# Optimization experiments

Hardware: AMD Instinct MI355X
Metric: run time of the kernel (lower is better)

The kernel has to match this reference:

```python
import jax, jax.numpy as jnp
import numpy as np

B, T, NS, NC, M = 256, 128, 12, 4, 6
MU = 0.1                 # barrier parameter alg.mu
REG_BASE = 1.6           # fp.reg_exp_base
REG = 2.0                # bp.reg
REG_FAC = REG_BASE ** REG - 1.0


def _mt(a):
    return jnp.swapaxes(a, -1, -2)


def setup_inputs():
    key = jax.random.key(0)
    k = jax.random.split(key, 18)
    rn = lambda i, shape: jax.random.normal(k[i], shape, dtype=jnp.float32)
    eye_s = jnp.eye(NS, dtype=jnp.float32)
    eye_c = jnp.eye(NC, dtype=jnp.float32)
    fx = 0.9 * eye_s + 0.02 * rn(0, (B, T, NS, NS))
    fu = 0.1 * rn(1, (B, T, NS, NC))
    fxx = 0.01 * rn(2, (B, T, NS, NS, NS))
    fxu = 0.01 * rn(3, (B, T, NS, NS, NC))
    fuu = 0.01 * rn(4, (B, T, NS, NC, NC))
    qx = 0.1 * rn(5, (B, T, NS))
    qu = 0.1 * rn(6, (B, T, NC))
    Ax = 0.1 * rn(7, (B, T, NS, NS))
    qxx = eye_s + Ax @ _mt(Ax)            # PSD stage cost Hessian
    Au = 0.1 * rn(8, (B, T, NC, NC))
    quu = eye_c + Au @ _mt(Au)            # PD control Hessian
    qxu = 0.05 * rn(9, (B, T, NS, NC))
    cx = 0.1 * rn(10, (B, T, M, NS))
    cu = 0.1 * rn(11, (B, T, M, NC))
    # feasible iterate: c < 0 strictly, dual s > 0
    c = -(jax.random.uniform(k[12], (B, T, M), dtype=jnp.float32) + 0.1)
    s = 0.05 + 0.1 * jax.random.uniform(k[13], (B, T, M), dtype=jnp.float32)
    px = 0.1 * rn(14, (B, NS))
    P = 0.1 * rn(15, (B, NS, NS))
    pxx = eye_s + P @ _mt(P)              # PSD terminal Hessian
    return {"qx": qx, "qu": qu, "qxx": qxx, "qxu": qxu, "quu": quu,
            "fx": fx, "fu": fu, "fxx": fxx, "fxu": fxu, "fuu": fuu,
            "cx": cx, "cu": cu, "c": c, "s": s, "px": px, "pxx": pxx}


def _backward_pass(qx, qu, qxx, qxu, quu, fx, fu, fxx, fxu, fuu, cx, cu, c, s, px, pxx):
    """Feasible-branch ipddp Riccati backward recursion over T steps, batched over B."""
    Bsz = qx.shape[0]

    def step(carry, inp):
        Vx, Vxx, dV0, dV1, qu_err, mu_err = carry
        (qx_t, qu_t, qxx_t, qxu_t, quu_t, fx_t, fu_t,
         fxx_t, fxu_t, fuu_t, cx_t, cu_t, c_t, s_t) = inp
        s_col = s_t[..., None]                      # (B,M,1)
        c_col = c_t[..., None]                      # (B,M,1)
        # Q-function expansions
        Qx = qx_t[..., None] + _mt(cx_t) @ s_col + _mt(fx_t) @ Vx       # (B,NS,1)
        Qu = qu_t[..., None] + _mt(cu_t) @ s_col + _mt(fu_t) @ Vx       # (B,NC,1)
        fxV = _mt(fx_t) @ Vxx
        v = Vx[..., 0]                              # (B,NS)
        Qxx = qxx_t + fxV @ fx_t + jnp.einsum('bs,bsij->bij', v, fxx_t)
        Qxu = qxu_t + fxV @ fu_t + jnp.einsum('bs,bsij->bij', v, fxu_t)
        Quu = quu_t + _mt(fu_t) @ Vxx @ fu_t + jnp.einsum('bs,bsij->bij', v, fuu_t)
        Quu = 0.5 * (Quu + _mt(Quu))
        Quu_reg = Quu + quu_t * REG_FAC
        # interior-point (feasible) modifications
        r = s_col * c_col + MU                      # (B,M,1)
        cinv = 1.0 / c_col
        sc = (s_t / c_t)[..., None]                 # diag(SCinv) entries
        SCcu = sc * cu_t                            # SCinv @ cu
        SCcx = sc * cx_t                            # SCinv @ cx
        cuSCcu = _mt(cu_t) @ SCcu
        Qu = Qu - _mt(cu_t) @ (cinv * r)
        tempQux = _mt(Qxu) - _mt(cu_t) @ SCcx       # (B,NC,NS)
        rhs = jnp.concatenate([Qu, tempQux], axis=-1)   # (B,NC,1+NS)
        kK = -jnp.linalg.solve(Quu_reg - cuSCcu, rhs)
        ku = kK[..., :1]                            # (B,NC,1)
        Ku = kK[..., 1:]                            # (B,NC,NS)
        cuku = cu_t @ ku                            # (B,M,1)
        ks = (-cinv * (r + s_col * cuku))[..., 0]   # (B,M)
        Ks = -(sc * (cx_t + cu_t @ Ku))             # (B,M,NS)
        Quu2 = Quu - cuSCcu
        Qxu2 = _mt(tempQux)
        Qxx2 = Qxx - _mt(cx_t) @ SCcx
        Qx2 = Qx - _mt(cx_t) @ (cinv * r)
        dV0 = dV0 + (_mt(ku) @ Qu)[..., 0, 0]
        dV1 = dV1 + 0.5 * (_mt(ku) @ Quu2 @ ku)[..., 0, 0]
        QxuKu = Qxu2 @ Ku
        KtQ = _mt(Ku) @ Quu2
        Vx_new = Qx2 + _mt(Ku) @ Qu + KtQ @ ku + Qxu2 @ ku
        Vxx_new = Qxx2 + _mt(QxuKu) + QxuKu + KtQ @ Ku
        Vxx_new = 0.5 * (Vxx_new + _mt(Vxx_new))
        qu_err = jnp.maximum(qu_err, jnp.max(jnp.abs(Qu)))
        mu_err = jnp.maximum(mu_err, jnp.max(jnp.abs(r)))
        return (Vx_new, Vxx_new, dV0, dV1, qu_err, mu_err), (ku[..., 0], Ku, ks, Ks)

    xs = tuple(jnp.moveaxis(a, 1, 0) for a in
               (qx, qu, qxx, qxu, quu, fx, fu, fxx, fxu, fuu, cx, cu, c, s))
    zero = jnp.zeros((), jnp.float32)
    init = (px[..., None], pxx, jnp.zeros((Bsz,), jnp.float32),
            jnp.zeros((Bsz,), jnp.float32), zero, zero)
    carry, outs = jax.lax.scan(step, init, xs, reverse=True)
    Vx, Vxx, dV0, dV1, qu_err, mu_err = carry
    ku, Ku, ks, Ks = (jnp.moveaxis(o, 0, 1) for o in outs)
    dV = jnp.stack([dV0, dV1], axis=-1)             # (B,2)
    opterr = jnp.maximum(qu_err, mu_err)            # c_err == 0 in feasible branch
    return ku, Ku, ks, Ks, dV, opterr, Vx[..., 0], Vxx


def reference(qx, qu, qxx, qxu, quu, fx, fu, fxx, fxu, fuu, cx, cu, c, s, px, pxx):
    return _backward_pass(qx, qu, qxx, qxu, quu, fx, fu, fxx, fxu, fuu,
                          cx, cu, c, s, px, pxx)
```

## Files before the change

kernel.cpp:

```cpp
#include <hip/hip_runtime.h>
#include <cstdint>
#include <cstddef>

#define B_  256
#define T_  128

constexpr float MU_F      = 0.1f;
constexpr float REG_FAC_F = (float)(1.6 * 1.6 - 1.0);

#define OF_FX   0
#define OF_FU   144
#define OF_FXX  192
#define OF_FXU  1920
#define OF_FUU  2496
#define OF_QXX  2688
#define OF_QXU  2832
#define OF_QUU  2880
#define OF_QX   2896
#define OF_QU   2908
#define OF_CX   2912
#define OF_CU   2984
#define OF_C    3008
#define OF_S    3014
#define STG_N   3020

#define O_KU    0
#define O_KUBIG 131072
#define O_KS    1703936
#define O_KSBIG 1900544
#define O_DV    4259840
#define O_OPT   4260352
#define O_VX    4260353
#define O_VXX   4263425

__device__ __forceinline__ void gl_lds16(const float* g, float* l) {
    __builtin_amdgcn_global_load_lds((const __attribute__((address_space(1))) void*)g,
                                     (__attribute__((address_space(3))) void*)l, 16, 0, 0);
}
__device__ __forceinline__ void gl_lds4(const float* g, float* l) {
    __builtin_amdgcn_global_load_lds((const __attribute__((address_space(1))) void*)g,
                                     (__attribute__((address_space(3))) void*)l, 4, 0, 0);
}
__device__ __forceinline__ void wait_vm0() {
    asm volatile("s_waitcnt vmcnt(0)" ::: "memory");
}

__global__ __launch_bounds__(64) void ddp_backward(
    const float* __restrict__ qx,  const float* __restrict__ qu,
    const float* __restrict__ qxx, const float* __restrict__ qxu,
    const float* __restrict__ quu, const float* __restrict__ fx,
    const float* __restrict__ fu,  const float* __restrict__ fxx,
    const float* __restrict__ fxu, const float* __restrict__ fuu,
    const float* __restrict__ cx,  const float* __restrict__ cu,
    const float* __restrict__ c_,  const float* __restrict__ s_,
    const float* __restrict__ px,  const float* __restrict__ pxx,
    float* __restrict__ out, float* __restrict__ ws)
{
    const int lane = threadIdx.x;
    const int b    = blockIdx.x;

    __shared__ float stg[2][STG_N];
    __shared__ float sVx[12], sVxx[144];
    __shared__ float sfxV[144], sfuV[48];
    __shared__ float sQxx2[144], stQux[48], sGuu[16];
    __shared__ float sQxb[12], sQub[4], sQu[4], sQx2[12];
    __shared__ float sr[6], scinv[6], ssc[6], sscr[6];
    __shared__ float sKu[48], sku[4];
    __shared__ float sErr[2];

    float accDV0 = 0.f, accDV1 = 0.f, accQE = 0.f, accME = 0.f;

    const float* srcs[14] = {qx, qu, qxx, qxu, quu, fx, fu, fxx, fxu, fuu, cx, cu, c_, s_};

    auto stage_all = [&](float* dst, int tt) {
        const size_t bt = (size_t)b * T_ + tt;
        constexpr int ch_arr[22]  = {5,6,7,7,7,7,7,7,7,8,8,8,9,2,3,4,0,1,10,11,12,13};
        constexpr int ch_goff[22] = {0,0,0,256,512,768,1024,1280,1536,0,256,512,0,0,0,0,0,0,0,0,0,0};
        constexpr int ch_loff[22] = {OF_FX, OF_FU,
                                     OF_FXX, OF_FXX+256, OF_FXX+512, OF_FXX+768,
                                     OF_FXX+1024, OF_FXX+1280, OF_FXX+1536,
                                     OF_FXU, OF_FXU+256, OF_FXU+512,
                                     OF_FUU, OF_QXX, OF_QXU, OF_QUU, OF_QX, OF_QU,
                                     OF_CX, OF_CU, OF_C, OF_S};
        constexpr int ch_nb[22]   = {576,192,1024,1024,1024,1024,1024,1024,768,
                                     1024,1024,256,768,576,192,64,48,16,288,96,24,24};
        constexpr int sl[14]      = {12,4,144,48,16,144,48,1728,576,192,72,24,6,6};
        #pragma unroll
        for (int ci = 0; ci < 22; ++ci) {
            const float* g = srcs[ch_arr[ci]] + bt * (size_t)sl[ch_arr[ci]] + ch_goff[ci];
            float* l = dst + ch_loff[ci];
            if ((ch_nb[ci] & 15) == 0) {
                if (lane * 16 < ch_nb[ci]) gl_lds16(g + lane * 4, l);
            } else {
                if (lane * 4  < ch_nb[ci]) gl_lds4 (g + lane,     l);
            }
        }
    };

    for (int e = lane; e < 144; e += 64) sVxx[e] = pxx[(size_t)b * 144 + e];
    if (lane < 12) sVx[lane] = px[(size_t)b * 12 + lane];
    stage_all(stg[0], T_ - 1);
    wait_vm0();
    __syncthreads();

    int cur = 0;
    for (int t = T_ - 1; t >= 0; --t) {
        const float* S = stg[cur];
        if (t > 0) stage_all(stg[cur ^ 1], t - 1);
        const size_t bt = (size_t)b * T_ + t;

        {
            const float* wp; int wss; float* op; int k0;
            if (lane < 48) {
                const int i = lane >> 2; k0 = (lane & 3) * 3;
                wp = S + OF_FX + i; wss = 12; op = sfxV + i * 12 + k0;
            } else {
                const int a = (lane - 48) >> 2; k0 = ((lane - 48) & 3) * 3;
                wp = S + OF_FU + a; wss = 4;  op = sfuV + a * 12 + k0;
            }
            float a0 = 0.f, a1 = 0.f, a2 = 0.f;
            #pragma unroll
            for (int m = 0; m < 12; ++m) {
                const float w = wp[m * wss];
                const float* vp = sVxx + m * 12 + k0;
                a0 += w * vp[0]; a1 += w * vp[1]; a2 += w * vp[2];
            }
            op[0] = a0; op[1] = a1; op[2] = a2;
        }
        if (lane < 6) {
            const int k = lane;
            const float cc = S[OF_C + k], sv = S[OF_S + k];
            const float r  = sv * cc + MU_F;
            const float ci = 1.0f / cc;
            sr[k] = r; scinv[k] = ci; ssc[k] = sv * ci; sscr[k] = ci * r;
        } else if (lane < 22) {
            const float* cp; int cs; const float* fp; int fs; float bias; float* o;
            if (lane < 18) { const int i = lane - 6;  cp = S + OF_CX + i; cs = 12; fp = S + OF_FX + i; fs = 12; bias = S[OF_QX + i]; o = sQxb + i; }
            else           { const int a = lane - 18; cp = S + OF_CU + a; cs = 4;  fp = S + OF_FU + a; fs = 4;  bias = S[OF_QU + a]; o = sQub + a; }
            float acc = bias;
            #pragma unroll
            for (int k = 0; k < 6; ++k)  acc += cp[k * cs] * S[OF_S + k];
            #pragma unroll
            for (int m = 0; m < 12; ++m) acc += fp[m * fs] * sVx[m];
            *o = acc;
        }
        __syncthreads();

        {
            const float *wp; int wss; const float *op; int osk, osd;
            const float *pp; int pss, psd; const float *up; int uss;
            const float *vp; const float *bp; int bsd; float *outp;
            if (lane < 48) {
                const int i = lane >> 2, j0 = (lane & 3) * 3;
                wp = sfxV + i * 12;           wss = 1;
                op = S + OF_FX + j0;          osk = 12; osd = 1;
                pp = S + OF_FXX + i * 12 + j0; pss = 144; psd = 1;
                up = S + OF_CX + i;           uss = 12;
                vp = S + OF_CX + j0;
                bp = S + OF_QXX + i * 12 + j0; bsd = 1;
                outp = sQxx2 + i * 12 + j0;
            } else {
                const int a = (lane - 48) >> 2, i0 = ((lane - 48) & 3) * 3;
                wp = S + OF_FU + a;           wss = 4;
                op = sfxV + i0 * 12;          osk = 1;  osd = 12;
                pp = S + OF_FXU + i0 * 4 + a; pss = 48; psd = 4;
                up = S + OF_CU + a;           uss = 4;
                vp = S + OF_CX + i0;
                bp = S + OF_QXU + i0 * 4 + a; bsd = 4;
                outp = stQux + a * 12 + i0;
            }
            float e0 = bp[0], e1 = bp[bsd], e2 = bp[2 * bsd];
            #pragma unroll
            for (int k = 0; k < 12; ++k) {
                const float w = wp[k * wss];
                const float* o = op + k * osk;
                e0 += w * o[0]; e1 += w * o[osd]; e2 += w * o[2 * osd];
            }
            #pragma unroll
            for (int s2 = 0; s2 < 12; ++s2) {
                const float v = sVx[s2];
                const float* p = pp + s2 * pss;
                e0 += v * p[0]; e1 += v * p[psd]; e2 += v * p[2 * psd];
            }
            #pragma unroll
            for (int k = 0; k < 6; ++k) {
                const float tt = ssc[k] * up[k * uss];
                const float* v = vp + k * 12;
                e0 -= tt * v[0]; e1 -= tt * v[1]; e2 -= tt * v[2];
            }
            outp[0] = e0; outp[1] = e1; outp[2] = e2;
        }
        if (lane < 16) {
            const int a = lane >> 2, b2 = lane & 3;
            float acc = S[OF_QUU + lane];
            #pragma unroll
            for (int k = 0; k < 12; ++k)  acc += sfuV[a * 12 + k] * S[OF_FU + k * 4 + b2];
            #pragma unroll
            for (int s2 = 0; s2 < 12; ++s2) acc += sVx[s2] * S[OF_FUU + s2 * 16 + lane];
            #pragma unroll
            for (int k = 0; k < 6; ++k)   acc -= ssc[k] * S[OF_CU + k * 4 + a] * S[OF_CU + k * 4 + b2];
            sGuu[lane] = acc;
        } else if (lane < 32) {
            const float* cp; int cs; float bias; float* o;
            if (lane < 20) { const int a = lane - 16; cp = S + OF_CU + a; cs = 4;  bias = sQub[a]; o = sQu + a; }
            else           { const int i = lane - 20; cp = S + OF_CX + i; cs = 12; bias = sQxb[i]; o = sQx2 + i; }
            float acc = bias;
            #pragma unroll
            for (int k = 0; k < 6; ++k) acc -= cp[k * cs] * sscr[k];
            *o = acc;
        }
        __syncthreads();

        float q2v[16];
        {
            float m4[16];
            #pragma unroll
            for (int e = 0; e < 16; ++e) {
                const int a = e >> 2, b2 = e & 3;
                const float g = 0.5f * (sGuu[e] + sGuu[b2 * 4 + a]);
                q2v[e] = g;
                m4[e]  = g + S[OF_QUU + e] * REG_FAC_F;
            }
            const float i0  = 1.0f / m4[0];
            const float l10 = m4[4] * i0, l20 = m4[8] * i0, l30 = m4[12] * i0;
            float a11 = m4[5]  - l10 * m4[1], a12 = m4[6]  - l10 * m4[2], a13 = m4[7]  - l10 * m4[3];
            float a21 = m4[9]  - l20 * m4[1], a22 = m4[10] - l20 * m4[2], a23 = m4[11] - l20 * m4[3];
            float a31 = m4[13] - l30 * m4[1], a32 = m4[14] - l30 * m4[2], a33 = m4[15] - l30 * m4[3];
            const float i1  = 1.0f / a11;
            const float l21 = a21 * i1, l31 = a31 * i1;
            a22 -= l21 * a12; a23 -= l21 * a13;
            a32 -= l31 * a12; a33 -= l31 * a13;
            const float i2  = 1.0f / a22;
            const float l32 = a32 * i2;
            a33 -= l32 * a23;

            if (lane < 13) {
                const int ii = (lane == 0) ? 0 : (lane - 1);
                float r0, r1, r2, r3;
                if (lane == 0) { r0 = sQu[0]; r1 = sQu[1]; r2 = sQu[2]; r3 = sQu[3]; }
                else { r0 = stQux[ii]; r1 = stQux[12 + ii]; r2 = stQux[24 + ii]; r3 = stQux[36 + ii]; }
                const float y0 = r0;
                const float y1 = r1 - l10 * y0;
                const float y2 = r2 - l20 * y0 - l21 * y1;
                const float y3 = r3 - l30 * y0 - l31 * y1 - l32 * y2;
                float x3 = y3 / a33;
                float x2 = (y2 - a23 * x3) * i2;
                float x1 = (y1 - a12 * x2 - a13 * x3) * i1;
                float x0 = (y0 - m4[1] * x1 - m4[2] * x2 - m4[3] * x3) * i0;
                x0 = -x0; x1 = -x1; x2 = -x2; x3 = -x3;

                const int gst = (lane == 0) ? 1 : 12;
                float* lK = (lane == 0) ? sku : (sKu + ii);
                lK[0] = x0; lK[gst] = x1; lK[2 * gst] = x2; lK[3 * gst] = x3;
                float* gK = (lane == 0) ? (out + O_KU + bt * 4) : (out + O_KUBIG + bt * 48 + ii);
                gK[0] = x0; gK[gst] = x1; gK[2 * gst] = x2; gK[3 * gst] = x3;

                const float* w1p = (lane == 0) ? scinv : ssc;
                const float* bpp = (lane == 0) ? sr : (S + OF_CX + ii);
                const int    bst = (lane == 0) ? 1 : 12;
                float* gS = (lane == 0) ? (out + O_KS + bt * 6) : (out + O_KSBIG + bt * 72 + ii);
                #pragma unroll
                for (int k = 0; k < 6; ++k) {
                    const float tsum = S[OF_CU + k*4] * x0 + S[OF_CU + k*4 + 1] * x1
                                     + S[OF_CU + k*4 + 2] * x2 + S[OF_CU + k*4 + 3] * x3;
                    const float w2 = (lane == 0) ? S[OF_S + k] : 1.0f;
                    gS[k * gst] = -w1p[k] * (bpp[k * bst] + w2 * tsum);
                }
            }
        }
        __syncthreads();

        if (lane < 48) {
            const int i = lane >> 2, j0 = (lane & 3) * 3;
            float kcol[4], tq[4], kt[4];
            #pragma unroll
            for (int a2 = 0; a2 < 4; ++a2) { kcol[a2] = sKu[a2 * 12 + i]; tq[a2] = stQux[a2 * 12 + i]; }
            #pragma unroll
            for (int a2 = 0; a2 < 4; ++a2)
                kt[a2] = kcol[0] * q2v[a2] + kcol[1] * q2v[4 + a2] + kcol[2] * q2v[8 + a2] + kcol[3] * q2v[12 + a2];
            #pragma unroll
            for (int d = 0; d < 3; ++d) {
                const int j = j0 + d;
                float acc = 0.5f * (sQxx2[i * 12 + j] + sQxx2[j * 12 + i]);
                #pragma unroll
                for (int a2 = 0; a2 < 4; ++a2) {
                    const float kj = sKu[a2 * 12 + j];
                    acc += tq[a2] * kj + stQux[a2 * 12 + j] * kcol[a2] + kt[a2] * kj;
                }
                sVxx[i * 12 + j] = acc;
            }
        } else if (lane < 60) {
            const int i = lane - 48;
            const float kc0 = sKu[i], kc1 = sKu[12 + i], kc2 = sKu[24 + i], kc3 = sKu[36 + i];
            float acc = sQx2[i] + kc0 * sQu[0] + kc1 * sQu[1] + kc2 * sQu[2] + kc3 * sQu[3];
            #pragma unroll
            for (int a2 = 0; a2 < 4; ++a2) {
                const float kta = kc0 * q2v[a2] + kc1 * q2v[4 + a2] + kc2 * q2v[8 + a2] + kc3 * q2v[12 + a2];
                acc += (kta + stQux[a2 * 12 + i]) * sku[a2];
            }
            sVx[i] = acc;
        } else if (lane == 60) {
            accDV0 += sku[0] * sQu[0] + sku[1] * sQu[1] + sku[2] * sQu[2] + sku[3] * sQu[3];
        } else if (lane == 61) {
            float d = 0.f;
            #pragma unroll
            for (int a2 = 0; a2 < 4; ++a2) {
                float tb = q2v[a2 * 4] * sku[0] + q2v[a2 * 4 + 1] * sku[1]
                         + q2v[a2 * 4 + 2] * sku[2] + q2v[a2 * 4 + 3] * sku[3];
                d += sku[a2] * tb;
            }
            accDV1 += 0.5f * d;
        } else if (lane == 62) {
            float m = fabsf(sQu[0]);
            m = fmaxf(m, fabsf(sQu[1])); m = fmaxf(m, fabsf(sQu[2])); m = fmaxf(m, fabsf(sQu[3]));
            accQE = fmaxf(accQE, m);
        } else {
            float m = 0.f;
            #pragma unroll
            for (int k = 0; k < 6; ++k) m = fmaxf(m, fabsf(sr[k]));
            accME = fmaxf(accME, m);
        }
        wait_vm0();
        __syncthreads();
        cur ^= 1;
    }

    if (lane == 60) out[O_DV + b * 2 + 0] = accDV0;
    if (lane == 61) out[O_DV + b * 2 + 1] = accDV1;
    if (lane == 62) sErr[0] = accQE;
    if (lane == 63) sErr[1] = accME;
    __syncthreads();
    if (lane == 0) ws[b] = fmaxf(sErr[0], sErr[1]);
    if (lane < 12) out[O_VX + b * 12 + lane] = sVx[lane];
    for (int e = lane; e < 144; e += 64) out[O_VXX + (size_t)b * 144 + e] = sVxx[e];
}

__global__ __launch_bounds__(256) void opt_reduce(const float* __restrict__ ws,
                                                  float* __restrict__ out)
{
    float v = ws[threadIdx.x];
    #pragma unroll
    for (int o = 32; o > 0; o >>= 1) v = fmaxf(v, __shfl_down(v, o, 64));
    __shared__ float m[4];
    if ((threadIdx.x & 63) == 0) m[threadIdx.x >> 6] = v;
    __syncthreads();
    if (threadIdx.x == 0) out[O_OPT] = fmaxf(fmaxf(m[0], m[1]), fmaxf(m[2], m[3]));
}

extern "C" void kernel_launch(void* const* d_in, const int* in_sizes, int n_in,
                              void* d_out, int out_size, void* d_ws, size_t ws_size,
                              hipStream_t stream) {
    const float* qx  = (const float*)d_in[0];
    const float* qu  = (const float*)d_in[1];
    const float* qxx = (const float*)d_in[2];
    const float* qxu = (const float*)d_in[3];
    const float* quu = (const float*)d_in[4];
    const float* fx  = (const float*)d_in[5];
    const float* fu  = (const float*)d_in[6];
    const float* fxx = (const float*)d_in[7];
    const float* fxu = (const float*)d_in[8];
    const float* fuu = (const float*)d_in[9];
    const float* cx  = (const float*)d_in[10];
    const float* cu  = (const float*)d_in[11];
    const float* c_  = (const float*)d_in[12];
    const float* s_  = (const float*)d_in[13];
    const float* px  = (const float*)d_in[14];
    const float* pxx = (const float*)d_in[15];
    float* out = (float*)d_out;
    float* ws  = (float*)d_ws;

    hipLaunchKernelGGL(ddp_backward, dim3(B_), dim3(64), 0, stream,
                       qx, qu, qxx, qxu, quu, fx, fu, fxx, fxu, fuu,
                       cx, cu, c_, s_, px, pxx, out, ws);
    hipLaunchKernelGGL(opt_reduce, dim3(1), dim3(256), 0, stream, ws, out);
}
```

Measured before the change: 860.6 us.

## Prefetch second-order tensors into registers, vectorize contractions, drop block barriers

The per-step staging of all inputs into LDS through global_load_lds is replaced. Only the small matrices are staged, via register loads written to LDS at the end of each step. The large fxx/fxu/fuu slices are instead prefetched one step ahead into float4 registers and contracted with Vx directly. Work is repartitioned so lanes compute float4 rows, and the __syncthreads barriers are dropped on the basis that the 64-thread block is a single wavefront. This aims to cut LDS traffic, wait latency and barrier cost on the serial recursion. In exchange it raises register pressure and relies on implicit in-wave ordering of LDS accesses.

Measured after the change: 858.6 us. Within noise of the previous version (-0.2%).

```diff
diff --git a/kernel.cpp b/kernel.cpp
--- a/kernel.cpp
+++ b/kernel.cpp
@@ -8,21 +8,22 @@
 constexpr float MU_F      = 0.1f;
 constexpr float REG_FAC_F = (float)(1.6 * 1.6 - 1.0);
 
-#define OF_FX   0
-#define OF_FU   144
-#define OF_FXX  192
-#define OF_FXU  1920
-#define OF_FUU  2496
-#define OF_QXX  2688
-#define OF_QXU  2832
-#define OF_QUU  2880
-#define OF_QX   2896
-#define OF_QU   2908
-#define OF_CX   2912
-#define OF_CU   2984
-#define OF_C    3008
-#define OF_S    3014
-#define STG_N   3020
+typedef float float4v __attribute__((ext_vector_type(4)));
+
+__device__ __forceinline__ float4v splat(float x) { float4v r = {x, x, x, x}; return r; }
+
+#define SF_FX   0
+#define SF_FU   144
+#define SF_QXX  192
+#define SF_QXU  336
+#define SF_QUU  384
+#define SF_QX   400
+#define SF_QU   412
+#define SF_CX   416
+#define SF_CU   488
+#define SF_C    512
+#define SF_S    520
+#define STG_N   532
 
 #define O_KU    0
 #define O_KUBIG 131072
@@ -32,18 +33,6 @@
 #define O_OPT   4260352
 #define O_VX    4260353
 #define O_VXX   4263425
-
-__device__ __forceinline__ void gl_lds16(const float* g, float* l) {
-    __builtin_amdgcn_global_load_lds((const __attribute__((address_space(1))) void*)g,
-                                     (__attribute__((address_space(3))) void*)l, 16, 0, 0);
-}
-__device__ __forceinline__ void gl_lds4(const float* g, float* l) {
-    __builtin_amdgcn_global_load_lds((const __attribute__((address_space(1))) void*)g,
-                                     (__attribute__((address_space(3))) void*)l, 4, 0, 0);
-}
-__device__ __forceinline__ void wait_vm0() {
-    asm volatile("s_waitcnt vmcnt(0)" ::: "memory");
-}
 
 __global__ __launch_bounds__(64) void ddp_backward(
     const float* __restrict__ qx,  const float* __restrict__ qu,
@@ -58,158 +47,199 @@
 {
     const int lane = threadIdx.x;
     const int b    = blockIdx.x;
-
-    __shared__ float stg[2][STG_N];
-    __shared__ float sVx[12], sVxx[144];
-    __shared__ float sfxV[144], sfuV[48];
-    __shared__ float sQxx2[144], stQux[48], sGuu[16];
-    __shared__ float sQxb[12], sQub[4], sQu[4], sQx2[12];
+    const size_t bt0 = (size_t)b * T_ + (T_ - 1);
+
+    __shared__ __align__(16) float stg[2][STG_N];
+    __shared__ __align__(16) float sVxx[144], sfxV[144], sQxx2[144];
+    __shared__ __align__(16) float sfuV[48], stQux[48], sKu[48];
+    __shared__ __align__(16) float sGuu[16];
+    __shared__ float sVx[12], sQxb[12], sQub[4], sQu[4], sQx2[12];
     __shared__ float sr[6], scinv[6], ssc[6], sscr[6];
-    __shared__ float sKu[48], sku[4];
-    __shared__ float sErr[2];
+    __shared__ float sku[4], sErr[2];
 
     float accDV0 = 0.f, accDV1 = 0.f, accQE = 0.f, accME = 0.f;
 
-    const float* srcs[14] = {qx, qu, qxx, qxu, quu, fx, fu, fxx, fxu, fuu, cx, cu, c_, s_};
-
-    auto stage_all = [&](float* dst, int tt) {
-        const size_t bt = (size_t)b * T_ + tt;
-        constexpr int ch_arr[22]  = {5,6,7,7,7,7,7,7,7,8,8,8,9,2,3,4,0,1,10,11,12,13};
-        constexpr int ch_goff[22] = {0,0,0,256,512,768,1024,1280,1536,0,256,512,0,0,0,0,0,0,0,0,0,0};
-        constexpr int ch_loff[22] = {OF_FX, OF_FU,
-                                     OF_FXX, OF_FXX+256, OF_FXX+512, OF_FXX+768,
-                                     OF_FXX+1024, OF_FXX+1280, OF_FXX+1536,
-                                     OF_FXU, OF_FXU+256, OF_FXU+512,
-                                     OF_FUU, OF_QXX, OF_QXU, OF_QUU, OF_QX, OF_QU,
-                                     OF_CX, OF_CU, OF_C, OF_S};
-        constexpr int ch_nb[22]   = {576,192,1024,1024,1024,1024,1024,1024,768,
-                                     1024,1024,256,768,576,192,64,48,16,288,96,24,24};
-        constexpr int sl[14]      = {12,4,144,48,16,144,48,1728,576,192,72,24,6,6};
+    const float* srcs[12] = {qx, qu, qxx, qxu, quu, fx, fu, cx, cu, c_, s_, qx};
+
+    const int segStart[10] = {0, 36, 48, 84, 96, 100, 103, 104, 122, 128};
+    const int segArr[9]    = {5, 6, 2, 3, 4, 0, 1, 7, 8};
+    const int segStride[9] = {144, 48, 144, 48, 16, 12, 4, 72, 24};
+
+    const float* gp0 = nullptr; int gstr0 = 0;
+    const float* gp1 = nullptr; int gstr1 = 0;
+    {
         #pragma unroll
-        for (int ci = 0; ci < 22; ++ci) {
-            const float* g = srcs[ch_arr[ci]] + bt * (size_t)sl[ch_arr[ci]] + ch_goff[ci];
-            float* l = dst + ch_loff[ci];
-            if ((ch_nb[ci] & 15) == 0) {
-                if (lane * 16 < ch_nb[ci]) gl_lds16(g + lane * 4, l);
-            } else {
-                if (lane * 4  < ch_nb[ci]) gl_lds4 (g + lane,     l);
-            }
-        }
-    };
+        for (int g = 0; g < 9; ++g) {
+            if (lane >= segStart[g] && lane < segStart[g + 1]) {
+                gp0 = srcs[segArr[g]] + bt0 * (size_t)segStride[g] + (lane - segStart[g]) * 4;
+                gstr0 = segStride[g];
+            }
+            const int s1 = 64 + lane;
+            if (s1 >= segStart[g] && s1 < segStart[g + 1]) {
+                gp1 = srcs[segArr[g]] + bt0 * (size_t)segStride[g] + (s1 - segStart[g]) * 4;
+                gstr1 = segStride[g];
+            }
+        }
+    }
+    const float* tp = (lane < 6) ? (c_ + bt0 * 6 + lane) : (s_ + bt0 * 6 + (lane - 6));
+    const int tailLds = (lane < 6) ? (SF_C + lane) : (SF_S + lane - 6);
+
+    const float* pfp; int pfStr; int pfSlice;
+    if (lane < 36) {
+        const int i = lane / 3, j0 = (lane % 3) * 4;
+        pfp = fxx + bt0 * 1728 + i * 12 + j0; pfStr = 144; pfSlice = 1728;
+    } else if (lane < 48) {
+        const int i = lane - 36;
+        pfp = fxu + bt0 * 576 + i * 4; pfStr = 48; pfSlice = 576;
+    } else if (lane < 52) {
+        const int a = lane - 48;
+        pfp = fuu + bt0 * 192 + a * 4; pfStr = 16; pfSlice = 192;
+    } else {
+        pfp = fuu + bt0 * 192; pfStr = 0; pfSlice = 0;
+    }
+    float4v pf[12];
 
     for (int e = lane; e < 144; e += 64) sVxx[e] = pxx[(size_t)b * 144 + e];
     if (lane < 12) sVx[lane] = px[(size_t)b * 12 + lane];
-    stage_all(stg[0], T_ - 1);
-    wait_vm0();
-    __syncthreads();
+    {
+        float4v g0 = *(const float4v*)gp0;
+        float4v g1 = *(const float4v*)gp1;
+        float gt = 0.f;
+        if (lane < 12) gt = *tp;
+        *(float4v*)&stg[0][4 * lane]       = g0;
+        *(float4v*)&stg[0][256 + 4 * lane] = g1;
+        if (lane < 12) stg[0][tailLds] = gt;
+        if (lane < 52) {
+            const float* p = pfp;
+            #pragma unroll
+            for (int s2 = 0; s2 < 12; ++s2) { pf[s2] = *(const float4v*)p; p += pfStr; }
+        }
+    }
 
     int cur = 0;
     for (int t = T_ - 1; t >= 0; --t) {
         const float* S = stg[cur];
-        if (t > 0) stage_all(stg[cur ^ 1], t - 1);
         const size_t bt = (size_t)b * T_ + t;
 
-        {
-            const float* wp; int wss; float* op; int k0;
-            if (lane < 48) {
-                const int i = lane >> 2; k0 = (lane & 3) * 3;
-                wp = S + OF_FX + i; wss = 12; op = sfxV + i * 12 + k0;
-            } else {
-                const int a = (lane - 48) >> 2; k0 = ((lane - 48) & 3) * 3;
-                wp = S + OF_FU + a; wss = 4;  op = sfuV + a * 12 + k0;
-            }
-            float a0 = 0.f, a1 = 0.f, a2 = 0.f;
-            #pragma unroll
-            for (int m = 0; m < 12; ++m) {
-                const float w = wp[m * wss];
-                const float* vp = sVxx + m * 12 + k0;
-                a0 += w * vp[0]; a1 += w * vp[1]; a2 += w * vp[2];
-            }
-            op[0] = a0; op[1] = a1; op[2] = a2;
-        }
-        if (lane < 6) {
-            const int k = lane;
-            const float cc = S[OF_C + k], sv = S[OF_S + k];
-            const float r  = sv * cc + MU_F;
+        float4v g0n, g1n; float gtn = 0.f;
+        if (t > 0) {
+            gp0 -= gstr0; gp1 -= gstr1;
+            g0n = *(const float4v*)gp0;
+            g1n = *(const float4v*)gp1;
+            if (lane < 12) { tp -= 6; gtn = *tp; }
+        }
+
+        if (lane < 36) {
+            const int i = lane / 3, k0 = (lane % 3) * 4;
+            float4v acc = splat(0.f);
+            #pragma unroll
+            for (int m = 0; m < 12; ++m)
+                acc += splat(S[SF_FX + m * 12 + i]) * (*(const float4v*)&sVxx[m * 12 + k0]);
+            *(float4v*)&sfxV[i * 12 + k0] = acc;
+        }
+        if (lane >= 36 && lane < 48) {
+            const int l = lane - 36, a = l / 3, k0 = (l % 3) * 4;
+            float4v acc = splat(0.f);
+            #pragma unroll
+            for (int m = 0; m < 12; ++m)
+                acc += splat(S[SF_FU + m * 4 + a]) * (*(const float4v*)&sVxx[m * 12 + k0]);
+            *(float4v*)&sfuV[a * 12 + k0] = acc;
+        }
+        if (lane >= 48 && lane < 54) {
+            const int k = lane - 48;
+            const float cc = S[SF_C + k], sv = S[SF_S + k];
+            const float r = sv * cc + MU_F;
             const float ci = 1.0f / cc;
             sr[k] = r; scinv[k] = ci; ssc[k] = sv * ci; sscr[k] = ci * r;
-        } else if (lane < 22) {
-            const float* cp; int cs; const float* fp; int fs; float bias; float* o;
-            if (lane < 18) { const int i = lane - 6;  cp = S + OF_CX + i; cs = 12; fp = S + OF_FX + i; fs = 12; bias = S[OF_QX + i]; o = sQxb + i; }
-            else           { const int a = lane - 18; cp = S + OF_CU + a; cs = 4;  fp = S + OF_FU + a; fs = 4;  bias = S[OF_QU + a]; o = sQub + a; }
-            float acc = bias;
-            #pragma unroll
-            for (int k = 0; k < 6; ++k)  acc += cp[k * cs] * S[OF_S + k];
-            #pragma unroll
-            for (int m = 0; m < 12; ++m) acc += fp[m * fs] * sVx[m];
-            *o = acc;
-        }
-        __syncthreads();
-
-        {
-            const float *wp; int wss; const float *op; int osk, osd;
-            const float *pp; int pss, psd; const float *up; int uss;
-            const float *vp; const float *bp; int bsd; float *outp;
-            if (lane < 48) {
-                const int i = lane >> 2, j0 = (lane & 3) * 3;
-                wp = sfxV + i * 12;           wss = 1;
-                op = S + OF_FX + j0;          osk = 12; osd = 1;
-                pp = S + OF_FXX + i * 12 + j0; pss = 144; psd = 1;
-                up = S + OF_CX + i;           uss = 12;
-                vp = S + OF_CX + j0;
-                bp = S + OF_QXX + i * 12 + j0; bsd = 1;
-                outp = sQxx2 + i * 12 + j0;
-            } else {
-                const int a = (lane - 48) >> 2, i0 = ((lane - 48) & 3) * 3;
-                wp = S + OF_FU + a;           wss = 4;
-                op = sfxV + i0 * 12;          osk = 1;  osd = 12;
-                pp = S + OF_FXU + i0 * 4 + a; pss = 48; psd = 4;
-                up = S + OF_CU + a;           uss = 4;
-                vp = S + OF_CX + i0;
-                bp = S + OF_QXU + i0 * 4 + a; bsd = 4;
-                outp = stQux + a * 12 + i0;
-            }
-            float e0 = bp[0], e1 = bp[bsd], e2 = bp[2 * bsd];
-            #pragma unroll
-            for (int k = 0; k < 12; ++k) {
-                const float w = wp[k * wss];
-                const float* o = op + k * osk;
-                e0 += w * o[0]; e1 += w * o[osd]; e2 += w * o[2 * osd];
-            }
-            #pragma unroll
-            for (int s2 = 0; s2 < 12; ++s2) {
-                const float v = sVx[s2];
-                const float* p = pp + s2 * pss;
-                e0 += v * p[0]; e1 += v * p[psd]; e2 += v * p[2 * psd];
-            }
+        }
+        if (lane >= 54 && lane < 58) {
+            const int a = lane - 54;
+            float acc = S[SF_QU + a];
+            #pragma unroll
+            for (int k = 0; k < 6; ++k)  acc += S[SF_CU + k * 4 + a] * S[SF_S + k];
+            #pragma unroll
+            for (int m = 0; m < 12; ++m) acc += S[SF_FU + m * 4 + a] * sVx[m];
+            sQub[a] = acc;
+        }
+        if (lane >= 52) {
+            const int i = lane - 52;
+            float acc = S[SF_QX + i];
+            #pragma unroll
+            for (int k = 0; k < 6; ++k)  acc += S[SF_CX + k * 12 + i] * S[SF_S + k];
+            #pragma unroll
+            for (int m = 0; m < 12; ++m) acc += S[SF_FX + m * 12 + i] * sVx[m];
+            sQxb[i] = acc;
+        }
+
+        if (lane < 36) {
+            const int i = lane / 3, j0 = (lane % 3) * 4;
+            float4v e = *(const float4v*)&S[SF_QXX + i * 12 + j0];
+            #pragma unroll
+            for (int k = 0; k < 12; ++k)
+                e += splat(sfxV[i * 12 + k]) * (*(const float4v*)&S[SF_FX + k * 12 + j0]);
+            #pragma unroll
+            for (int s2 = 0; s2 < 12; ++s2) e += splat(sVx[s2]) * pf[s2];
             #pragma unroll
             for (int k = 0; k < 6; ++k) {
-                const float tt = ssc[k] * up[k * uss];
-                const float* v = vp + k * 12;
-                e0 -= tt * v[0]; e1 -= tt * v[1]; e2 -= tt * v[2];
-            }
-            outp[0] = e0; outp[1] = e1; outp[2] = e2;
-        }
-        if (lane < 16) {
-            const int a = lane >> 2, b2 = lane & 3;
-            float acc = S[OF_QUU + lane];
-            #pragma unroll
-            for (int k = 0; k < 12; ++k)  acc += sfuV[a * 12 + k] * S[OF_FU + k * 4 + b2];
-            #pragma unroll
-            for (int s2 = 0; s2 < 12; ++s2) acc += sVx[s2] * S[OF_FUU + s2 * 16 + lane];
-            #pragma unroll
-            for (int k = 0; k < 6; ++k)   acc -= ssc[k] * S[OF_CU + k * 4 + a] * S[OF_CU + k * 4 + b2];
-            sGuu[lane] = acc;
-        } else if (lane < 32) {
-            const float* cp; int cs; float bias; float* o;
-            if (lane < 20) { const int a = lane - 16; cp = S + OF_CU + a; cs = 4;  bias = sQub[a]; o = sQu + a; }
-            else           { const int i = lane - 20; cp = S + OF_CX + i; cs = 12; bias = sQxb[i]; o = sQx2 + i; }
-            float acc = bias;
-            #pragma unroll
-            for (int k = 0; k < 6; ++k) acc -= cp[k * cs] * sscr[k];
-            *o = acc;
-        }
-        __syncthreads();
+                const float tt = ssc[k] * S[SF_CX + k * 12 + i];
+                e -= splat(tt) * (*(const float4v*)&S[SF_CX + k * 12 + j0]);
+            }
+            *(float4v*)&sQxx2[i * 12 + j0] = e;
+        }
+        if (lane >= 36 && lane < 48) {
+            const int i = lane - 36;
+            float4v e = *(const float4v*)&S[SF_QXU + i * 4];
+            #pragma unroll
+            for (int k = 0; k < 12; ++k)
+                e += splat(sfxV[i * 12 + k]) * (*(const float4v*)&S[SF_FU + k * 4]);
+            #pragma unroll
+            for (int s2 = 0; s2 < 12; ++s2) e += splat(sVx[s2]) * pf[s2];
+            #pragma unroll
+            for (int k = 0; k < 6; ++k) {
+                const float tt = ssc[k] * S[SF_CX + k * 12 + i];
+                e -= splat(tt) * (*(const float4v*)&S[SF_CU + k * 4]);
+            }
+            stQux[i]      = e.x;
+            stQux[12 + i] = e.y;
+            stQux[24 + i] = e.z;
+            stQux[36 + i] = e.w;
+        }
+        if (lane >= 48 && lane < 52) {
+            const int a = lane - 48;
+            float4v g = *(const float4v*)&S[SF_QUU + a * 4];
+            #pragma unroll
+            for (int k = 0; k < 12; ++k)
+                g += splat(sfuV[a * 12 + k]) * (*(const float4v*)&S[SF_FU + k * 4]);
+            #pragma unroll
+            for (int s2 = 0; s2 < 12; ++s2) g += splat(sVx[s2]) * pf[s2];
+            #pragma unroll
+            for (int k = 0; k < 6; ++k) {
+                const float tt = ssc[k] * S[SF_CU + k * 4 + a];
+                g -= splat(tt) * (*(const float4v*)&S[SF_CU + k * 4]);
+            }
+            *(float4v*)&sGuu[a * 4] = g;
+        }
+        if (lane >= 52 && lane < 56) {
+            const int a = lane - 52;
+            float acc = sQub[a];
+            #pragma unroll
+            for (int k = 0; k < 6; ++k) acc -= S[SF_CU + k * 4 + a] * sscr[k];
+            sQu[a] = acc;
+        }
+        if (lane >= 52) {
+            const int i = lane - 52;
+            float acc = sQxb[i];
+            #pragma unroll
+            for (int k = 0; k < 6; ++k) acc -= S[SF_CX + k * 12 + i] * sscr[k];
+            sQx2[i] = acc;
+        }
+
+        if (t > 0 && lane < 52) {
+            pfp -= pfSlice;
+            const float* p = pfp;
+            #pragma unroll
+            for (int s2 = 0; s2 < 12; ++s2) { pf[s2] = *(const float4v*)p; p += pfStr; }
+        }
 
         float q2v[16];
         {
@@ -217,9 +247,9 @@
             #pragma unroll
             for (int e = 0; e < 16; ++e) {
                 const int a = e >> 2, b2 = e & 3;
-                const float g = 0.5f * (sGuu[e] + sGuu[b2 * 4 + a]);
-                q2v[e] = g;
-                m4[e]  = g + S[OF_QUU + e] * REG_FAC_F;
+                const float gv = 0.5f * (sGuu[e] + sGuu[b2 * 4 + a]);
+                q2v[e] = gv;
+                m4[e]  = gv + S[SF_QUU + e] * REG_FAC_F;
             }
             const float i0  = 1.0f / m4[0];
             const float l10 = m4[4] * i0, l20 = m4[8] * i0, l30 = m4[12] * i0;
@@ -256,19 +286,17 @@
                 gK[0] = x0; gK[gst] = x1; gK[2 * gst] = x2; gK[3 * gst] = x3;
 
                 const float* w1p = (lane == 0) ? scinv : ssc;
-                const float* bpp = (lane == 0) ? sr : (S + OF_CX + ii);
-                const int    bst = (lane == 0) ? 1 : 12;
                 float* gS = (lane == 0) ? (out + O_KS + bt * 6) : (out + O_KSBIG + bt * 72 + ii);
                 #pragma unroll
                 for (int k = 0; k < 6; ++k) {
-                    const float tsum = S[OF_CU + k*4] * x0 + S[OF_CU + k*4 + 1] * x1
-                                     + S[OF_CU + k*4 + 2] * x2 + S[OF_CU + k*4 + 3] * x3;
-                    const float w2 = (lane == 0) ? S[OF_S + k] : 1.0f;
-                    gS[k * gst] = -w1p[k] * (bpp[k * bst] + w2 * tsum);
+                    const float tsum = S[SF_CU + k * 4] * x0 + S[SF_CU + k * 4 + 1] * x1
+                                     + S[SF_CU + k * 4 + 2] * x2 + S[SF_CU + k * 4 + 3] * x3;
+                    const float bv = (lane == 0) ? sr[k] : S[SF_CX + k * 12 + ii];
+                    const float w2 = (lane == 0) ? S[SF_S + k] : 1.0f;
+                    gS[k * gst] = -w1p[k] * (bv + w2 * tsum);
                 }
             }
         }
-        __syncthreads();
 
         if (lane < 48) {
             const int i = lane >> 2, j0 = (lane & 3) * 3;
@@ -320,8 +348,13 @@
             for (int k = 0; k < 6; ++k) m = fmaxf(m, fabsf(sr[k]));
             accME = fmaxf(accME, m);
         }
-        wait_vm0();
-        __syncthreads();
+
+        if (t > 0) {
+            float* D = stg[cur ^ 1];
+            *(float4v*)&D[4 * lane]       = g0n;
+            *(float4v*)&D[256 + 4 * lane] = g1n;
+            if (lane < 12) D[tailLds] = gtn;
+        }
         cur ^= 1;
     }
 
```
